# Kernel tuning notes

Hardware: AMD Instinct MI355X
Metric: run time of the kernel (lower is better)

## Reference

```python
import jax, jax.numpy as jnp
import numpy as np

B, H, S, D = 4, 16, 2048, 64
SCALE = 8.0  # sqrt(D)
NEG = -1000000000.0


def setup_inputs() -> dict:
    key = jax.random.key(0)
    kq, kk, kv = jax.random.split(key, 3)
    q = jax.random.normal(kq, (B, H, S, D), dtype=jnp.float32)
    k = jax.random.normal(kk, (B, H, S, D), dtype=jnp.float32)
    v = jax.random.normal(kv, (B, H, S, D), dtype=jnp.float32)
    # causal mask: True means masked out (matches torch masked_fill)
    mask = jnp.triu(jnp.ones((S, S), dtype=bool), k=1)[None, None, :, :]
    mask = jnp.broadcast_to(mask, (B, 1, S, S))
    return {"q": q, "k": k, "v": v, "mask": mask}


def reference(q, k, v, mask):
    # score = q @ k^T / scale  -> [B,H,S,S]
    score = jnp.einsum("bhqd,bhkd->bhqk", q, k) / SCALE
    score = jnp.where(mask, NEG, score)
    probs = jax.nn.softmax(score, axis=-1)
    context = jnp.einsum("bhqk,bhkd->bhqd", probs, v)
    return context
```

## Files before the change

### kernel.cpp

```cpp
#include <hip/hip_runtime.h>

#define SQ 2048
#define DH 64
#define BK 64
#define NQT 32
#define NBH 64
#define M0 8.0f

#define WS_BYTES ((size_t)2 * NBH * SQ * DH * 2)

typedef float f32x4 __attribute__((ext_vector_type(4)));
typedef __bf16 bf16x8 __attribute__((ext_vector_type(8)));
typedef _Float16 f16x4 __attribute__((ext_vector_type(4)));
typedef __fp16 fp16x2 __attribute__((ext_vector_type(2)));
typedef unsigned short u16x8 __attribute__((ext_vector_type(8)));
typedef unsigned int u32x4 __attribute__((ext_vector_type(4)));

static __device__ __forceinline__ unsigned int pkbf(float a, float b) {
#if __has_builtin(__builtin_amdgcn_cvt_pk_bf16_f32)
  typedef __bf16 bf16x2 __attribute__((ext_vector_type(2)));
  bf16x2 r = __builtin_amdgcn_cvt_pk_bf16_f32(a, b);
  return __builtin_bit_cast(unsigned int, r);
#else
  unsigned int ua = __builtin_bit_cast(unsigned int, a);
  unsigned int ub = __builtin_bit_cast(unsigned int, b);
  ua += 0x7fffu + ((ua >> 16) & 1u);
  ub += 0x7fffu + ((ub >> 16) & 1u);
  return (ua >> 16) | (ub & 0xffff0000u);
#endif
}

static __device__ __forceinline__ unsigned int pkf16(float a, float b) {
  fp16x2 r = __builtin_amdgcn_cvt_pkrtz(a, b);
  return __builtin_bit_cast(unsigned int, r);
}

static __device__ __forceinline__ f32x4 mfma_qk(u16x8 a, u16x8 b, f32x4 c) {
  return __builtin_amdgcn_mfma_f32_16x16x32_bf16(
      __builtin_bit_cast(bf16x8, a), __builtin_bit_cast(bf16x8, b), c, 0, 0, 0);
}

static __device__ __forceinline__ f32x4 mfma_pv(f16x4 a, f16x4 b, f32x4 c) {
  return __builtin_amdgcn_mfma_f32_16x16x16f16(a, b, c, 0, 0, 0);
}

static __device__ __forceinline__ void ld16(unsigned short* l, const unsigned short* g) {
  __builtin_amdgcn_global_load_lds(
      (const __attribute__((address_space(1))) unsigned int*)(const void*)g,
      (__attribute__((address_space(3))) unsigned int*)(void*)l, 16, 0, 0);
}

static __device__ __forceinline__ void store_tile(float* wb, float* dst,
                                                  const f32x4* o, int lane,
                                                  int l15, int quad) {
#pragma unroll
  for (int dt = 0; dt < 4; ++dt) {
    const int colw = dt * 16 + quad * 4;
    *(f32x4*)&wb[l15 * 64 + (colw ^ ((l15 & 3) * 16))] = o[dt];
  }
  __builtin_amdgcn_wave_barrier();
#pragma unroll
  for (int j = 0; j < 4; ++j) {
    const int row = j * 4 + (lane >> 4);
    const int colw = (lane & 15) * 4;
    f32x4 v = *(const f32x4*)&wb[row * 64 + (colw ^ ((row & 3) * 16))];
    *(f32x4*)&dst[row * 64 + colw] = v;
  }
}

__global__ __launch_bounds__(256) void prep(const float* __restrict__ K,
                                            const float* __restrict__ V,
                                            unsigned short* __restrict__ Kb,
                                            unsigned short* __restrict__ Vt) {
  const int bh = (int)blockIdx.x >> 5;
  const int st = (int)blockIdx.x & 31;
  const int tid = threadIdx.x;
  __shared__ __align__(16) unsigned short T[DH * 64];
  {
    const int r = tid >> 2, c0 = (tid & 3) * 16;
    const float* kp = K + ((size_t)bh * SQ + st * 64 + r) * DH + c0;
    f32x4 x0 = *(const f32x4*)kp, x1 = *(const f32x4*)(kp + 4),
          x2 = *(const f32x4*)(kp + 8), x3 = *(const f32x4*)(kp + 12);
    u32x4 w0 = {pkbf(x0[0], x0[1]), pkbf(x0[2], x0[3]), pkbf(x1[0], x1[1]), pkbf(x1[2], x1[3])};
    u32x4 w1 = {pkbf(x2[0], x2[1]), pkbf(x2[2], x2[3]), pkbf(x3[0], x3[1]), pkbf(x3[2], x3[3])};
    unsigned short* kb = Kb + ((size_t)bh * SQ + st * 64 + r) * DH + c0;
    *(u32x4*)kb = w0;
    *(u32x4*)(kb + 8) = w1;
  }
  {
    const int kvb = (tid >> 4) * 4, vdb = (tid & 15) * 4;
    const float* vp = V + ((size_t)bh * SQ + st * 64 + kvb) * DH + vdb;
    f32x4 r0 = *(const f32x4*)vp, r1 = *(const f32x4*)(vp + DH),
          r2 = *(const f32x4*)(vp + 2 * DH), r3 = *(const f32x4*)(vp + 3 * DH);
    const int uu = kvb >> 3, h = (kvb >> 2) & 1;
#pragma unroll
    for (int i = 0; i < 4; ++i) {
      const int d = vdb + i;
      uint2 w = {pkf16(r0[i], r1[i]), pkf16(r2[i], r3[i])};
      *(uint2*)&T[d * 64 + ((uu ^ (d & 7)) * 8) + h * 4] = w;
    }
  }
  __syncthreads();
  {
    const int d2 = tid >> 2, cp = (tid & 3) * 2;
#pragma unroll
    for (int e = 0; e < 2; ++e) {
      const int uu = cp + e;
      u16x8 val = *(const u16x8*)&T[d2 * 64 + ((uu ^ (d2 & 7)) * 8)];
      *(u16x8*)&Vt[(size_t)bh * DH * SQ + (size_t)d2 * SQ + st * 64 + uu * 8] = val;
    }
  }
}

__global__ __launch_bounds__(256, 4) void fa_main(
    const float* __restrict__ Q, const unsigned short* __restrict__ Kb,
    const unsigned short* __restrict__ Vt, float* __restrict__ O) {
  const int lin = (int)blockIdx.x;
  const int xcd = lin & 7, u = lin >> 3, hh = u & 7, p = u >> 3;
  const int bh = hh * 8 + xcd;
  const int qtl = p, qth = NQT - 1 - p;

  const int tid = threadIdx.x;
  const int wv = tid >> 6;
  const int lane = tid & 63;
  const int l15 = lane & 15;
  const int quad = lane >> 4;

  __shared__ __align__(16) unsigned short S0[2 * BK * DH];
  __shared__ __align__(16) unsigned short S1[2 * BK * DH];

  const size_t hq = (size_t)bh * (SQ * DH);
  const unsigned short* KbH = Kb + (size_t)bh * SQ * DH;
  const unsigned short* VtH = Vt + (size_t)bh * DH * SQ;

  const int srow = wv * 16 + (lane >> 3);
  const int sc = lane & 7;

  u16x8 qfl[2], qfh[2];
  {
    const float scq = 0.125f * 1.4426950408889634f;
#pragma unroll
    for (int g = 0; g < 2; ++g) {
      const int wq0 = (g ? qth : qtl) * 64 + wv * 16;
      const float* qp = Q + hq + (size_t)(wq0 + l15) * DH + quad * 8;
#pragma unroll
      for (int c = 0; c < 2; ++c) {
        f32x4 x = *(const f32x4*)(qp + c * 32);
        f32x4 y = *(const f32x4*)(qp + c * 32 + 4);
        u32x4 w = {pkbf(x[0] * scq, x[1] * scq), pkbf(x[2] * scq, x[3] * scq),
                   pkbf(y[0] * scq, y[1] * scq), pkbf(y[2] * scq, y[3] * scq)};
        (g ? qfh : qfl)[c] = __builtin_bit_cast(u16x8, w);
      }
    }
  }

  f32x4 ol[4], oh[4];
#pragma unroll
  for (int dt = 0; dt < 4; ++dt) {
    ol[dt] = (f32x4){0.f, 0.f, 0.f, 0.f};
    oh[dt] = (f32x4){0.f, 0.f, 0.f, 0.f};
  }
  float ll = 0.f, lh = 0.f;

  auto stage = [&](unsigned short* W, int t) {
    const int kb = t * BK;
    unsigned short* Kd = W;
    unsigned short* Vd = W + BK * DH;
#pragma unroll
    for (int j = 0; j < 2; ++j) {
      const int row = srow + j * 8;
      ld16(&Kd[row * 64 + sc * 8], &KbH[(size_t)(kb + row) * 64 + ((sc ^ (row & 7)) * 8)]);
      ld16(&Vd[row * 64 + sc * 8], &VtH[(size_t)row * SQ + kb + ((sc ^ (row & 7)) * 8)]);
    }
  };

  auto attend = [&](const unsigned short* R, const u16x8* qf, f32x4* o,
                    float& lsum, bool diag) {
    const unsigned short* Ks = R;
    const unsigned short* Vs = R + BK * DH;
    f32x4 s[4];
#pragma unroll
    for (int nt = 0; nt < 4; ++nt) {
      f32x4 acc = {-M0, -M0, -M0, -M0};
#pragma unroll
      for (int c = 0; c < 2; ++c) {
        const int row = nt * 16 + l15;
        const int un = c * 4 + quad;
        u16x8 kf = *(const u16x8*)&Ks[row * 64 + ((un ^ (row & 7)) * 8)];
        acc = mfma_qk(kf, qf[c], acc);
      }
      s[nt] = acc;
    }
    if (diag) {
#pragma unroll
      for (int nt = 0; nt < 4; ++nt)
#pragma unroll
        for (int r = 0; r < 4; ++r)
          if (nt * 16 + quad * 4 + r > wv * 16 + l15) s[nt][r] = -1e30f;
    }
    f16x4 pf[4];
#pragma unroll
    for (int nt = 0; nt < 4; ++nt) {
      f32x4 pr;
#pragma unroll
      for (int r = 0; r < 4; ++r) {
        pr[r] = __builtin_amdgcn_exp2f(s[nt][r]);
        lsum += pr[r];
      }
      uint2 w2 = {pkf16(pr[0], pr[1]), pkf16(pr[2], pr[3])};
      pf[nt] = __builtin_bit_cast(f16x4, w2);
    }
#pragma unroll
    for (int dt = 0; dt < 4; ++dt) {
      const int d = dt * 16 + l15;
#pragma unroll
      for (int nt = 0; nt < 4; ++nt) {
        const int uv = nt * 2 + (quad >> 1);
        f16x4 vf = *(const f16x4*)&Vs[d * 64 + ((uv ^ (d & 7)) * 8) + (quad & 1) * 4];
        o[dt] = mfma_pv(vf, pf[nt], o[dt]);
      }
    }
  };

  auto step = [&](int t, const unsigned short* R, unsigned short* W) {
    if (t + 1 <= qth) stage(W, t + 1);
    if (t <= qtl) attend(R, qfl, ol, ll, t == qtl);
    attend(R, qfh, oh, lh, t == qth);
    __syncthreads();
  };

  stage(S0, 0);
  __syncthreads();
  for (int t = 0; t <= qth; t += 2) {
    step(t, S0, S1);
    if (t + 1 <= qth) step(t + 1, S1, S0);
  }

  ll += __shfl_xor(ll, 16, 64);
  ll += __shfl_xor(ll, 32, 64);
  lh += __shfl_xor(lh, 16, 64);
  lh += __shfl_xor(lh, 32, 64);
  float* wb = (float*)S0 + wv * 1024;
  {
    const float inv = 1.0f / ll;
    f32x4 on[4];
#pragma unroll
    for (int dt = 0; dt < 4; ++dt) on[dt] = ol[dt] * inv;
    store_tile(wb, O + hq + (size_t)(qtl * 64 + wv * 16) * DH, on, lane, l15, quad);
  }
  {
    const float inv = 1.0f / lh;
    f32x4 on[4];
#pragma unroll
    for (int dt = 0; dt < 4; ++dt) on[dt] = oh[dt] * inv;
    store_tile(wb, O + hq + (size_t)(qth * 64 + wv * 16) * DH, on, lane, l15, quad);
  }
}

__global__ __launch_bounds__(256, 4) void fa_full(
    const float* __restrict__ Q, const float* __restrict__ K,
    const float* __restrict__ V, float* __restrict__ O) {
  const int lin = (int)blockIdx.x;
  const int xcd = lin & 7;
  const int u = lin >> 3;
  const int hh = u & 7;
  const int p = u >> 3;
  const int bh = hh * 8 + xcd;
  const int tid = threadIdx.x;
  const int wv = tid >> 6;
  const int lane = tid & 63;
  const int l15 = lane & 15;
  const int quad = lane >> 4;
  __shared__ __align__(16) unsigned short SMEM[2][2 * BK * DH];
  const size_t hbase = (size_t)bh * (SQ * DH);
  const int krr = tid >> 3, kcc = (tid & 7) * 8;
  const int kvb = (tid >> 4) * 4, vdb = (tid & 15) * 4;
#pragma unroll
  for (int ph = 0; ph < 2; ++ph) {
    const int qt = ph ? (NQT - 1 - p) : p;
    const int wq0 = qt * 64 + wv * 16;
    u16x8 qf[2];
    {
      const float scq = 0.125f * 1.4426950408889634f;
      const float* qp = Q + hbase + (size_t)(wq0 + l15) * DH + quad * 8;
#pragma unroll
      for (int c = 0; c < 2; ++c) {
        f32x4 x = *(const f32x4*)(qp + c * 32);
        f32x4 y = *(const f32x4*)(qp + c * 32 + 4);
        u32x4 w = {pkbf(x[0] * scq, x[1] * scq), pkbf(x[2] * scq, x[3] * scq),
                   pkbf(y[0] * scq, y[1] * scq), pkbf(y[2] * scq, y[3] * scq)};
        qf[c] = __builtin_bit_cast(u16x8, w);
      }
    }
    f32x4 o[4];
#pragma unroll
    for (int dt = 0; dt < 4; ++dt) o[dt] = (f32x4){0.f, 0.f, 0.f, 0.f};
    float l = 0.f;
    f32x4 ka[2][2], va[4];
    {
      const float* kp = K + hbase + (size_t)krr * DH + kcc;
      ka[0][0] = *(const f32x4*)kp;             ka[0][1] = *(const f32x4*)(kp + 4);
      ka[1][0] = *(const f32x4*)(kp + 32 * DH); ka[1][1] = *(const f32x4*)(kp + 32 * DH + 4);
      const float* vp = V + hbase + (size_t)kvb * DH + vdb;
      va[0] = *(const f32x4*)vp;            va[1] = *(const f32x4*)(vp + DH);
      va[2] = *(const f32x4*)(vp + 2 * DH); va[3] = *(const f32x4*)(vp + 3 * DH);
    }
    __syncthreads();
    {
      unsigned short* Ksn = SMEM[0];
      unsigned short* Vsn = SMEM[0] + BK * DH;
#pragma unroll
      for (int h = 0; h < 2; ++h) {
        const int rr = h * 32 + krr;
        u32x4 w = {pkbf(ka[h][0][0], ka[h][0][1]), pkbf(ka[h][0][2], ka[h][0][3]),
                   pkbf(ka[h][1][0], ka[h][1][1]), pkbf(ka[h][1][2], ka[h][1][3])};
        *(u32x4*)&Ksn[rr * DH + (kcc ^ ((rr & 7) * 8))] = w;
      }
#pragma unroll
      for (int i = 0; i < 4; ++i) {
        const int d = vdb + i;
        uint2 w = {pkf16(va[0][i], va[1][i]), pkf16(va[2][i], va[3][i])};
        *(uint2*)&Vsn[d * BK + (kvb ^ ((d & 15) * 4))] = w;
      }
    }
    __syncthreads();
    for (int t = 0; t <= qt; ++t) {
      const unsigned short* Ks = SMEM[t & 1];
      const unsigned short* Vs = SMEM[t & 1] + BK * DH;
      if (t < qt) {
        const int kb2 = (t + 1) * BK;
        const float* kp = K + hbase + (size_t)(kb2 + krr) * DH + kcc;
        ka[0][0] = *(const f32x4*)kp;             ka[0][1] = *(const f32x4*)(kp + 4);
        ka[1][0] = *(const f32x4*)(kp + 32 * DH); ka[1][1] = *(const f32x4*)(kp + 32 * DH + 4);
        const float* vp = V + hbase + (size_t)(kb2 + kvb) * DH + vdb;
        va[0] = *(const f32x4*)vp;            va[1] = *(const f32x4*)(vp + DH);
        va[2] = *(const f32x4*)(vp + 2 * DH); va[3] = *(const f32x4*)(vp + 3 * DH);
      }
      f32x4 s[4];
#pragma unroll
      for (int nt = 0; nt < 4; ++nt) {
        f32x4 acc = {-M0, -M0, -M0, -M0};
#pragma unroll
        for (int c = 0; c < 2; ++c) {
          const int row = nt * 16 + l15;
          u16x8 kf = *(const u16x8*)&Ks[row * DH + ((c * 32 + quad * 8) ^ ((l15 & 7) * 8))];
          acc = mfma_qk(kf, qf[c], acc);
        }
        s[nt] = acc;
      }
      if (t == qt) {
#pragma unroll
        for (int nt = 0; nt < 4; ++nt)
#pragma unroll
          for (int r = 0; r < 4; ++r)
            if (nt * 16 + quad * 4 + r > wv * 16 + l15) s[nt][r] = -1e30f;
      }
      f16x4 pf[4];
#pragma unroll
      for (int nt = 0; nt < 4; ++nt) {
        f32x4 pr;
#pragma unroll
        for (int r = 0; r < 4; ++r) { pr[r] = __builtin_amdgcn_exp2f(s[nt][r]); l += pr[r]; }
        uint2 w2 = {pkf16(pr[0], pr[1]), pkf16(pr[2], pr[3])};
        pf[nt] = __builtin_bit_cast(f16x4, w2);
      }
#pragma unroll
      for (int dt = 0; dt < 4; ++dt) {
        const int d = dt * 16 + l15;
#pragma unroll
        for (int nt = 0; nt < 4; ++nt) {
          f16x4 vf = *(const f16x4*)&Vs[d * BK + ((nt * 16 + quad * 4) ^ (l15 * 4))];
          o[dt] = mfma_pv(vf, pf[nt], o[dt]);
        }
      }
      if (t < qt) {
        unsigned short* Ksn = SMEM[(t + 1) & 1];
        unsigned short* Vsn = SMEM[(t + 1) & 1] + BK * DH;
#pragma unroll
        for (int h = 0; h < 2; ++h) {
          const int rr = h * 32 + krr;
          u32x4 w = {pkbf(ka[h][0][0], ka[h][0][1]), pkbf(ka[h][0][2], ka[h][0][3]),
                     pkbf(ka[h][1][0], ka[h][1][1]), pkbf(ka[h][1][2], ka[h][1][3])};
          *(u32x4*)&Ksn[rr * DH + (kcc ^ ((rr & 7) * 8))] = w;
        }
#pragma unroll
        for (int i = 0; i < 4; ++i) {
          const int d = vdb + i;
          uint2 w = {pkf16(va[0][i], va[1][i]), pkf16(va[2][i], va[3][i])};
          *(uint2*)&Vsn[d * BK + (kvb ^ ((d & 15) * 4))] = w;
        }
        __syncthreads();
      }
    }
    l += __shfl_xor(l, 16, 64);
    l += __shfl_xor(l, 32, 64);
    const float inv = 1.0f / l;
    f32x4 on[4];
#pragma unroll
    for (int dt = 0; dt < 4; ++dt) on[dt] = o[dt] * inv;
    float* wb = (float*)SMEM[(qt + 1) & 1] + wv * 1024;
    store_tile(wb, O + hbase + (size_t)wq0 * DH, on, lane, l15, quad);
  }
}

extern "C" void kernel_launch(void* const* d_in, const int* in_sizes, int n_in,
                              void* d_out, int out_size, void* d_ws, size_t ws_size,
                              hipStream_t stream) {
  const float* q = (const float*)d_in[0];
  const float* k = (const float*)d_in[1];
  const float* v = (const float*)d_in[2];
  float* o = (float*)d_out;
  if (ws_size >= WS_BYTES) {
    unsigned short* Kb = (unsigned short*)d_ws;
    unsigned short* Vt = Kb + (size_t)NBH * SQ * DH;
    prep<<<dim3(NBH * 32), 256, 0, stream>>>(k, v, Kb, Vt);
    fa_main<<<dim3(1024), 256, 0, stream>>>(q, Kb, Vt, o);
  } else {
    fa_full<<<dim3(1024), 256, 0, stream>>>(q, k, v, o);
  }
}
```

Measured before the change: 216.6 us.

## Compute softmax row sums with MFMA and deepen K/V prefetch to two tiles

The staging schedule changes so each LDS buffer is refilled right after the barrier that follows its use, with tile t+2 loaded. The load for the next tile is issued a full iteration ahead, which gives global-to-LDS copies more time to overlap with compute. The per-lane scalar accumulation of exp values and the final cross-lane shuffles are replaced by an extra MFMA per score tile that multiplies the probabilities by a ones vector. This moves the row-sum work from VALU to the matrix unit, at the cost of a few more MFMA instructions and two extra accumulator registers.

```diff
diff --git a/kernel.cpp b/kernel.cpp
--- a/kernel.cpp
+++ b/kernel.cpp
@@ -154,13 +154,15 @@
     }
   }
 
-  f32x4 ol[4], oh[4];
+  f32x4 ol[4], oh[4], lal, lah;
 #pragma unroll
   for (int dt = 0; dt < 4; ++dt) {
     ol[dt] = (f32x4){0.f, 0.f, 0.f, 0.f};
     oh[dt] = (f32x4){0.f, 0.f, 0.f, 0.f};
   }
-  float ll = 0.f, lh = 0.f;
+  lal = (f32x4){0.f, 0.f, 0.f, 0.f};
+  lah = (f32x4){0.f, 0.f, 0.f, 0.f};
+  const f16x4 ones = {(_Float16)1.f, (_Float16)1.f, (_Float16)1.f, (_Float16)1.f};
 
   auto stage = [&](unsigned short* W, int t) {
     const int kb = t * BK;
@@ -175,7 +177,7 @@
   };
 
   auto attend = [&](const unsigned short* R, const u16x8* qf, f32x4* o,
-                    float& lsum, bool diag) {
+                    f32x4& la, bool diag) {
     const unsigned short* Ks = R;
     const unsigned short* Vs = R + BK * DH;
     f32x4 s[4];
@@ -203,13 +205,12 @@
     for (int nt = 0; nt < 4; ++nt) {
       f32x4 pr;
 #pragma unroll
-      for (int r = 0; r < 4; ++r) {
-        pr[r] = __builtin_amdgcn_exp2f(s[nt][r]);
-        lsum += pr[r];
-      }
+      for (int r = 0; r < 4; ++r) pr[r] = __builtin_amdgcn_exp2f(s[nt][r]);
       uint2 w2 = {pkf16(pr[0], pr[1]), pkf16(pr[2], pr[3])};
       pf[nt] = __builtin_bit_cast(f16x4, w2);
     }
+#pragma unroll
+    for (int nt = 0; nt < 4; ++nt) la = mfma_pv(ones, pf[nt], la);
 #pragma unroll
     for (int dt = 0; dt < 4; ++dt) {
       const int d = dt * 16 + l15;
@@ -223,33 +224,30 @@
   };
 
   auto step = [&](int t, const unsigned short* R, unsigned short* W) {
-    if (t + 1 <= qth) stage(W, t + 1);
-    if (t <= qtl) attend(R, qfl, ol, ll, t == qtl);
-    attend(R, qfh, oh, lh, t == qth);
+    if (t <= qtl) attend(R, qfl, ol, lal, t == qtl);
+    attend(R, qfh, oh, lah, t == qth);
     __syncthreads();
+    if (t + 2 <= qth) stage(W, t + 2);
   };
 
   stage(S0, 0);
   __syncthreads();
+  stage(S1, 1);
   for (int t = 0; t <= qth; t += 2) {
-    step(t, S0, S1);
-    if (t + 1 <= qth) step(t + 1, S1, S0);
-  }
-
-  ll += __shfl_xor(ll, 16, 64);
-  ll += __shfl_xor(ll, 32, 64);
-  lh += __shfl_xor(lh, 16, 64);
-  lh += __shfl_xor(lh, 32, 64);
+    step(t, S0, S0);
+    if (t + 1 <= qth) step(t + 1, S1, S1);
+  }
+
   float* wb = (float*)S0 + wv * 1024;
   {
-    const float inv = 1.0f / ll;
+    const float inv = 1.0f / lal[0];
     f32x4 on[4];
 #pragma unroll
     for (int dt = 0; dt < 4; ++dt) on[dt] = ol[dt] * inv;
     store_tile(wb, O + hq + (size_t)(qtl * 64 + wv * 16) * DH, on, lane, l15, quad);
   }
   {
-    const float inv = 1.0f / lh;
+    const float inv = 1.0f / lah[0];
     f32x4 on[4];
 #pragma unroll
     for (int dt = 0; dt < 4; ++dt) on[dt] = oh[dt] * inv;
```

After: 217.8 us. No clear change (+0.6%).
